# Kernel tuning notes

Measured on AMD Instinct MI355X. Metric: run time of the kernel, lower is better.

## Reference

```python
import jax, jax.numpy as jnp
import numpy as np

N = 16384   # nodes = batch(4) * 64*64 grid
E = 32768   # edges per edge set
L = 32      # LATENT_DIMS
D = 2       # DEPTH (message-passing layers per GNOBlock)
KD = 64     # KERNEL_DIMS
TIN = 10    # TIME_STEPS_IN

def gelu(x):
    return jax.nn.gelu(x, approximate=False)  # torch F.gelu default (erf)

def setup_inputs() -> dict:
    key = jax.random.key(0)
    ks = iter(jax.random.split(key, 64))
    def nrm(shape, s=0.1):
        return jax.random.normal(next(ks), shape, dtype=jnp.float32) * s
    def ridx():
        return jax.random.randint(next(ks), (2, E), 0, N)
    inp = {
        'nodes': nrm((N, TIN), 1.0),
        'grid': jax.random.uniform(next(ks), (N, 2), dtype=jnp.float32),
    }
    for nm in ['11', '12', '22', '23', '33', '32', '21']:
        inp[f'edge_index_{nm}'] = ridx()
    for nm in ['11', '12', '22', '23', '33', '32', '21']:
        inp[f'edge_attr_{nm}'] = nrm((E, 5), 1.0)
    inp['batch_size'] = 4
    inp['image_size'] = 64
    # projector MLP: in_dims=TIN+2 -> hidden L//2 -> L
    inp['proj_w1'] = nrm((TIN + 2, L // 2)); inp['proj_b1'] = jnp.zeros((L // 2,), jnp.float32)
    inp['proj_w2'] = nrm((L // 2, L));       inp['proj_b2'] = jnp.zeros((L,), jnp.float32)
    # decoder MLP: L -> L//2 -> 1
    inp['dec_w1'] = nrm((L, L // 2)); inp['dec_b1'] = jnp.zeros((L // 2,), jnp.float32)
    inp['dec_w2'] = nrm((L // 2, 1)); inp['dec_b2'] = jnp.zeros((1,), jnp.float32)
    # 7 GNOBlocks x D layers: edge kernel MLP (5 -> KD -> L*L) + node linear (L -> L)
    inp['kw1'] = nrm((7, D, 5, KD));      inp['kb1'] = jnp.zeros((7, D, KD), jnp.float32)
    inp['kw2'] = nrm((7, D, KD, L * L));  inp['kb2'] = jnp.zeros((7, D, L * L), jnp.float32)
    inp['lw'] = nrm((7, D, L, L));        inp['lb'] = jnp.zeros((7, D, L), jnp.float32)
    return inp

def _mlp(x, w1, b1, w2, b2):
    return gelu(x @ w1 + b1) @ w2 + b2

def _gno_block(i, x, eidx, eattr, kw1, kb1, kw2, kb2, lw, lb):
    src, dst = eidx[0], eidx[1]
    n = x.shape[0]
    deg = jax.ops.segment_sum(jnp.ones_like(dst, x.dtype), dst, num_segments=n)
    inv_deg = jnp.where(deg > 0, 1.0 / jnp.maximum(deg, 1.0), 0.0)[:, None]
    for d in range(kw1.shape[1]):
        # edge-conditioned kernel: [E, L, L]
        k = _mlp(eattr, kw1[i, d], kb1[i, d], kw2[i, d], kb2[i, d]).reshape(-1, x.shape[1], x.shape[1])
        msg = jnp.einsum('eio,ei->eo', k, x[src])            # gather + per-edge matvec
        agg = jax.ops.segment_sum(msg, dst, num_segments=n) * inv_deg  # scatter-mean
        x = gelu(x @ lw[i, d] + lb[i, d] + agg)              # root linear + activation
    return x

def reference(nodes, grid, edge_index_11, edge_index_12, edge_index_22, edge_index_23,
              edge_index_33, edge_index_32, edge_index_21, edge_attr_11, edge_attr_12,
              edge_attr_22, edge_attr_23, edge_attr_33, edge_attr_32, edge_attr_21,
              batch_size, image_size, proj_w1, proj_b1, proj_w2, proj_b2,
              dec_w1, dec_b1, dec_w2, dec_b2, kw1, kb1, kw2, kb2, lw, lb):
    x = jnp.concatenate([nodes, grid], axis=-1)
    x = gelu(_mlp(x, proj_w1, proj_b1, proj_w2, proj_b2))
    # block param index order matches init order: k11,k22,k33,k12,k23,k32,k21
    n11 = _gno_block(0, x, edge_index_11, edge_attr_11, kw1, kb1, kw2, kb2, lw, lb)
    n12 = _gno_block(3, x, edge_index_12, edge_attr_12, kw1, kb1, kw2, kb2, lw, lb)
    n22 = _gno_block(1, n12, edge_index_22, edge_attr_22, kw1, kb1, kw2, kb2, lw, lb)
    n23 = _gno_block(4, n12, edge_index_23, edge_attr_23, kw1, kb1, kw2, kb2, lw, lb)
    n33 = _gno_block(2, n23, edge_index_33, edge_attr_33, kw1, kb1, kw2, kb2, lw, lb)
    n32 = _gno_block(5, n33, edge_index_32, edge_attr_32, kw1, kb1, kw2, kb2, lw, lb)
    n21 = _gno_block(6, n32 + n22, edge_index_21, edge_attr_21, kw1, kb1, kw2, kb2, lw, lb)
    out = _mlp(n21 + n11, dec_w1, dec_b1, dec_w2, dec_b2)
    return out
```

## Files before the change

kernel.cpp:

```cpp
#include <hip/hip_runtime.h>

#define Nn 16384
#define Ee 32768
#define NL (Nn * 32)

typedef _Float16 hf16;
typedef _Float16 half8 __attribute__((ext_vector_type(8)));
typedef float f32x16 __attribute__((ext_vector_type(16)));

__device__ __forceinline__ float gelu_f(float x) {
    return 0.5f * x * (1.0f + erff(x * 0.7071067811865476f));
}

__device__ __forceinline__ f32x16 zero16() {
    f32x16 v;
#pragma unroll
    for (int r = 0; r < 16; ++r) v[r] = 0.0f;
    return v;
}

__global__ __launch_bounds__(256) void proj_kernel(
    const float* __restrict__ nodes, const float* __restrict__ grid2,
    const float* __restrict__ w1, const float* __restrict__ b1,
    const float* __restrict__ w2, const float* __restrict__ b2,
    float* __restrict__ x0, int* __restrict__ deg_i, int* __restrict__ cursor)
{
    const int n = blockIdx.x * 256 + threadIdx.x;
    float in[12];
#pragma unroll
    for (int j = 0; j < 10; ++j) in[j] = nodes[n * 10 + j];
    in[10] = grid2[n * 2 + 0];
    in[11] = grid2[n * 2 + 1];
    float h[16];
#pragma unroll
    for (int j = 0; j < 16; ++j) {
        float a = b1[j];
#pragma unroll
        for (int i = 0; i < 12; ++i) a = fmaf(in[i], w1[i * 16 + j], a);
        h[j] = gelu_f(a);
    }
#pragma unroll
    for (int o = 0; o < 32; ++o) {
        float a = b2[o];
#pragma unroll
        for (int j = 0; j < 16; ++j) a = fmaf(h[j], w2[j * 32 + o], a);
        x0[(size_t)n * 32 + o] = gelu_f(a);
    }
#pragma unroll
    for (int s = 0; s < 7; ++s) { deg_i[s * Nn + n] = 0; cursor[s * Nn + n] = 0; }
}

struct EPtrs { const int* p[7]; };

__global__ __launch_bounds__(256) void count_deg_kernel(EPtrs ei, int* __restrict__ deg_i)
{
    const int t = blockIdx.x * 256 + threadIdx.x;
    const int s = t >> 15;
    const int e = t & (Ee - 1);
    const int dst = ei.p[s][Ee + e];
    atomicAdd(&deg_i[s * Nn + dst], 1);
}

__global__ __launch_bounds__(256) void scan_kernel(const int* __restrict__ deg_i,
                                                   int* __restrict__ off)
{
    const int s = blockIdx.x;
    const int t = threadIdx.x;
    const int* d = deg_i + (size_t)s * Nn;
    int* o = off + (size_t)s * (Nn + 1);
    int local[64];
    int sum = 0;
#pragma unroll
    for (int j = 0; j < 64; ++j) { local[j] = d[t * 64 + j]; sum += local[j]; }
    __shared__ int ps[256];
    ps[t] = sum;
    __syncthreads();
    for (int st = 1; st < 256; st <<= 1) {
        int v = (t >= st) ? ps[t - st] : 0;
        __syncthreads();
        ps[t] += v;
        __syncthreads();
    }
    int base = (t > 0) ? ps[t - 1] : 0;
#pragma unroll
    for (int j = 0; j < 64; ++j) { o[t * 64 + j] = base; base += local[j]; }
    if (t == 255) o[Nn] = base;
}

__global__ __launch_bounds__(256) void rank_kernel(EPtrs ei, const int* __restrict__ off,
                                                   int* __restrict__ cursor,
                                                   int* __restrict__ rank)
{
    const int t = blockIdx.x * 256 + threadIdx.x;
    const int s = t >> 15;
    const int e = t & (Ee - 1);
    const int dst = ei.p[s][Ee + e];
    const int r = off[(size_t)s * (Nn + 1) + dst] + atomicAdd(&cursor[s * Nn + dst], 1);
    rank[(size_t)s * Ee + e] = r;
}

__global__ __launch_bounds__(320) void wprep_kernel(const float* __restrict__ kw2,
                                                    const float* __restrict__ kb2,
                                                    hf16* __restrict__ Wpack)
{
    const int id = blockIdx.x >> 5;
    const int nt = blockIdx.x & 31;
    const int t = threadIdx.x;
    const int ks = t >> 6, lane = t & 63;
    const float* kw2l = kw2 + (size_t)id * 65536;
    const float* kb2l = kb2 + (size_t)id * 1024;
    half8 vh, vl;
#pragma unroll
    for (int j = 0; j < 8; ++j) {
        const int k = ks * 16 + (lane >> 5) * 8 + j;
        float v = 0.0f;
        if (ks < 4) v = kw2l[(size_t)k * 1024 + (lane & 31) * 32 + nt];
        else if (k == 64) v = kb2l[(lane & 31) * 32 + nt];
        const hf16 h = (hf16)v;
        vh[j] = h;
        vl[j] = (hf16)((v - (float)h) * 1024.0f);
    }
    half8* dst = (half8*)(Wpack + ((size_t)(id * 32 + nt) * 10 + ks * 2) * 512);
    dst[0 * 64 + lane] = vh;
    dst[1 * 64 + lane] = vl;
}

__global__ __launch_bounds__(256, 2) void gemm_kernel(
    const float* __restrict__ xa, const float* __restrict__ xb,
    const int* __restrict__ esrc, const int* __restrict__ erank,
    const float* __restrict__ eattr,
    const float* __restrict__ kw1l, const float* __restrict__ kb1l,
    const hf16* __restrict__ WpackL,
    float* __restrict__ msgS)
{
    __shared__ __align__(16) hf16 hLDS[4 * 5 * 2 * 512];
    const int eblk = blockIdx.x >> 1;
    const int hf = blockIdx.x & 1;
    const int t = threadIdx.x, l = t & 63, wv = t >> 6;
    half8* hp8 = (half8*)hLDS;

    {
        const int e_loc = t >> 1;
        const int hpart = t & 1;
        const int mt = e_loc >> 5, colbase = e_loc & 31;
        const int eg = eblk * 128 + e_loc;
        float ea5[5];
#pragma unroll
        for (int j = 0; j < 5; ++j) ea5[j] = eattr[(size_t)eg * 5 + j];
        half8 vh[2][2], vl[2][2];
#pragma unroll
        for (int hh = 0; hh < 32; ++hh) {
            const int h = hpart * 32 + hh;
            float pre = kb1l[h];
#pragma unroll
            for (int j = 0; j < 5; ++j) pre = fmaf(ea5[j], kw1l[j * 64 + h], pre);
            const float H = gelu_f(pre);
            const hf16 hv = (hf16)H;
            vh[hh >> 4][(hh >> 3) & 1][hh & 7] = hv;
            vl[hh >> 4][(hh >> 3) & 1][hh & 7] = (hf16)((H - (float)hv) * 1024.0f);
        }
#pragma unroll
        for (int ksl = 0; ksl < 2; ++ksl)
#pragma unroll
            for (int kh = 0; kh < 2; ++kh) {
                const int f = (mt * 5 + hpart * 2 + ksl) * 2;
                hp8[f * 64 + colbase + kh * 32] = vh[ksl][kh];
                hp8[(f + 1) * 64 + colbase + kh * 32] = vl[ksl][kh];
            }
        if (hpart == 0) {
            half8 oneV, zV;
#pragma unroll
            for (int j = 0; j < 8; ++j) { oneV[j] = (hf16)0.0f; zV[j] = (hf16)0.0f; }
            oneV[0] = (hf16)1.0f;
            const int f4 = (mt * 5 + 4) * 2;
            hp8[f4 * 64 + colbase] = oneV;
            hp8[f4 * 64 + colbase + 32] = zV;
            hp8[(f4 + 1) * 64 + colbase] = zV;
            hp8[(f4 + 1) * 64 + colbase + 32] = zV;
        }
    }

    const int hi = l >> 5;
    const int el = eblk * 128 + wv * 32 + (l & 31);
    const int src = esrc[el];
    const int rk = erank[el];
    float xsr[16];
#pragma unroll
    for (int c = 0; c < 4; ++c) {
        float4 v = *reinterpret_cast<const float4*>(xa + (size_t)src * 32 + c * 8 + hi * 4);
        if (xb) {
            float4 u = *reinterpret_cast<const float4*>(xb + (size_t)src * 32 + c * 8 + hi * 4);
            v.x += u.x; v.y += u.y; v.z += u.z; v.w += u.w;
        }
        xsr[c * 4 + 0] = v.x; xsr[c * 4 + 1] = v.y;
        xsr[c * 4 + 2] = v.z; xsr[c * 4 + 3] = v.w;
    }

    __syncthreads();

    half8 Hh[5], Hl[5];
#pragma unroll
    for (int ks = 0; ks < 5; ++ks) {
        Hh[ks] = hp8[((wv * 5 + ks) * 2 + 0) * 64 + l];
        Hl[ks] = hp8[((wv * 5 + ks) * 2 + 1) * 64 + l];
    }

    float4 p4;
    const hf16* wbase = WpackL + (size_t)hf * 16 * 5120;

#define LOADW(TT, WH, WL) { \
    const half8* wp = (const half8*)(wbase + (size_t)(TT) * 5120); \
    _Pragma("unroll") for (int ks = 0; ks < 5; ++ks) { \
        WH[ks] = wp[(ks * 2 + 0) * 64 + l]; \
        WL[ks] = wp[(ks * 2 + 1) * 64 + l]; } }

#define COMPUTE(TT, WH, WL) { \
    f32x16 ah = zero16(), ax = zero16(); \
    _Pragma("unroll") for (int ks = 0; ks < 5; ++ks) { \
        ah = __builtin_amdgcn_mfma_f32_32x32x16_f16(WH[ks], Hh[ks], ah, 0, 0, 0); \
        ax = __builtin_amdgcn_mfma_f32_32x32x16_f16(WL[ks], Hh[ks], ax, 0, 0, 0); \
        ax = __builtin_amdgcn_mfma_f32_32x32x16_f16(WH[ks], Hl[ks], ax, 0, 0, 0); } \
    float ph = 0.0f, px = 0.0f; \
    _Pragma("unroll") for (int r = 0; r < 16; ++r) { \
        ph = fmaf(ah[r], xsr[r], ph); px = fmaf(ax[r], xsr[r], px); } \
    float p = fmaf(px, 9.765625e-4f, ph); \
    p += __shfl_xor(p, 32); \
    p4[(TT) & 3] = p; \
    if (((TT) & 3) == 3 && l < 32) \
        *reinterpret_cast<float4*>(msgS + (size_t)rk * 32 + hf * 16 + ((TT) - 3)) = p4; }

    half8 WhA[5], WlA[5], WhB[5], WlB[5];
    LOADW(0, WhA, WlA)
#pragma unroll
    for (int g = 0; g < 8; ++g) {
        LOADW(2 * g + 1, WhB, WlB)
        COMPUTE(2 * g, WhA, WlA)
        if (g < 7) LOADW(2 * g + 2, WhA, WlA)
        COMPUTE(2 * g + 1, WhB, WlB)
    }
#undef LOADW
#undef COMPUTE
}

__global__ __launch_bounds__(256) void node_update_kernel(
    const float* __restrict__ xa, const float* __restrict__ xb,
    float* __restrict__ xout, const float* __restrict__ msgS,
    const int* __restrict__ off,
    const float* __restrict__ lw, const float* __restrict__ lb)
{
    __shared__ float lwS[1024];
#pragma unroll
    for (int c = 0; c < 4; ++c) lwS[threadIdx.x + 256 * c] = lw[threadIdx.x + 256 * c];
    __syncthreads();

    const int g = blockIdx.x * 256 + threadIdx.x;
    const int n = g >> 2;
    const int q = g & 3;

    const int b = off[n], e = off[n + 1];
    float sum[8];
#pragma unroll
    for (int oo = 0; oo < 8; ++oo) sum[oo] = 0.0f;
    for (int j = b; j < e; ++j) {
        const float4 m0 = *reinterpret_cast<const float4*>(msgS + (size_t)j * 32 + q * 8);
        const float4 m1 = *reinterpret_cast<const float4*>(msgS + (size_t)j * 32 + q * 8 + 4);
        sum[0] += m0.x; sum[1] += m0.y; sum[2] += m0.z; sum[3] += m0.w;
        sum[4] += m1.x; sum[5] += m1.y; sum[6] += m1.z; sum[7] += m1.w;
    }
    const float inv = (e > b) ? 1.0f / (float)(e - b) : 0.0f;
    float acc[8];
#pragma unroll
    for (int oo = 0; oo < 8; ++oo) acc[oo] = fmaf(sum[oo], inv, lb[q * 8 + oo]);

    float row[32];
#pragma unroll
    for (int i = 0; i < 32; i += 4) {
        float4 v = *reinterpret_cast<const float4*>(xa + (size_t)n * 32 + i);
        if (xb) {
            float4 u = *reinterpret_cast<const float4*>(xb + (size_t)n * 32 + i);
            v.x += u.x; v.y += u.y; v.z += u.z; v.w += u.w;
        }
        row[i + 0] = v.x; row[i + 1] = v.y; row[i + 2] = v.z; row[i + 3] = v.w;
    }
#pragma unroll
    for (int i = 0; i < 32; ++i) {
        const float xi = row[i];
#pragma unroll
        for (int oo = 0; oo < 8; ++oo) acc[oo] = fmaf(xi, lwS[i * 32 + q * 8 + oo], acc[oo]);
    }
    float4 o0, o1;
    o0.x = gelu_f(acc[0]); o0.y = gelu_f(acc[1]); o0.z = gelu_f(acc[2]); o0.w = gelu_f(acc[3]);
    o1.x = gelu_f(acc[4]); o1.y = gelu_f(acc[5]); o1.z = gelu_f(acc[6]); o1.w = gelu_f(acc[7]);
    *reinterpret_cast<float4*>(xout + (size_t)n * 32 + q * 8) = o0;
    *reinterpret_cast<float4*>(xout + (size_t)n * 32 + q * 8 + 4) = o1;
}

__global__ __launch_bounds__(256) void decode_kernel(
    const float* __restrict__ a, const float* __restrict__ b,
    const float* __restrict__ w1, const float* __restrict__ b1,
    const float* __restrict__ w2, const float* __restrict__ b2,
    float* __restrict__ out)
{
    const int n = blockIdx.x * 256 + threadIdx.x;
    float s[32];
#pragma unroll
    for (int i = 0; i < 32; ++i) s[i] = a[(size_t)n * 32 + i] + b[(size_t)n * 32 + i];
    float acc = b2[0];
#pragma unroll
    for (int j = 0; j < 16; ++j) {
        float h = b1[j];
#pragma unroll
        for (int i = 0; i < 32; ++i) h = fmaf(s[i], w1[i * 16 + j], h);
        acc = fmaf(gelu_f(h), w2[j], acc);
    }
    out[n] = acc;
}

extern "C" void kernel_launch(void* const* d_in, const int* in_sizes, int n_in,
                              void* d_out, int out_size, void* d_ws, size_t ws_size,
                              hipStream_t stream)
{
    const float* nodes = (const float*)d_in[0];
    const float* grid2 = (const float*)d_in[1];
    const int* ei[7];
    const float* ea[7];
    for (int s = 0; s < 7; ++s) {
        ei[s] = (const int*)d_in[2 + s];
        ea[s] = (const float*)d_in[9 + s];
    }
    const float* pw1 = (const float*)d_in[18];
    const float* pb1 = (const float*)d_in[19];
    const float* pw2 = (const float*)d_in[20];
    const float* pb2 = (const float*)d_in[21];
    const float* dw1 = (const float*)d_in[22];
    const float* db1 = (const float*)d_in[23];
    const float* dw2 = (const float*)d_in[24];
    const float* db2 = (const float*)d_in[25];
    const float* kw1 = (const float*)d_in[26];
    const float* kb1 = (const float*)d_in[27];
    const float* kw2 = (const float*)d_in[28];
    const float* kb2 = (const float*)d_in[29];
    const float* lw  = (const float*)d_in[30];
    const float* lb  = (const float*)d_in[31];

    float* ws  = (float*)d_ws;
    float* x0   = ws + 0 * (size_t)NL;
    float* n11  = ws + 1 * (size_t)NL;
    float* n12  = ws + 2 * (size_t)NL;
    float* n22  = ws + 3 * (size_t)NL;
    float* n23  = ws + 4 * (size_t)NL;
    float* n33  = ws + 5 * (size_t)NL;
    float* n32  = ws + 6 * (size_t)NL;
    float* n21  = ws + 7 * (size_t)NL;
    float* msgS = ws + 8 * (size_t)NL;
    size_t cur = 8 * (size_t)NL + (size_t)Ee * 32;
    hf16* Wpack = (hf16*)(ws + cur);
    cur += (size_t)14 * 32 * 10 * 512 / 2;
    int* deg_i  = (int*)(ws + cur); cur += (size_t)7 * Nn;
    int* cursor = (int*)(ws + cur); cur += (size_t)7 * Nn;
    int* off    = (int*)(ws + cur); cur += (size_t)7 * (Nn + 1);
    int* rank   = (int*)(ws + cur);

    proj_kernel<<<Nn / 256, 256, 0, stream>>>(nodes, grid2, pw1, pb1, pw2, pb2,
                                              x0, deg_i, cursor);

    EPtrs ep;
    for (int s = 0; s < 7; ++s) ep.p[s] = ei[s];
    count_deg_kernel<<<7 * Ee / 256, 256, 0, stream>>>(ep, deg_i);
    scan_kernel<<<7, 256, 0, stream>>>(deg_i, off);
    rank_kernel<<<7 * Ee / 256, 256, 0, stream>>>(ep, off, cursor, rank);
    wprep_kernel<<<14 * 32, 320, 0, stream>>>(kw2, kb2, Wpack);

    auto layer = [&](int i, int d, int s, const float* xa, const float* xb, float* xo) {
        const int id = i * 2 + d;
        gemm_kernel<<<(Ee / 128) * 2, 256, 0, stream>>>(
            xa, xb, ei[s], rank + (size_t)s * Ee, ea[s],
            kw1 + (size_t)id * 320, kb1 + (size_t)id * 64,
            Wpack + (size_t)id * 32 * 5120, msgS);
        node_update_kernel<<<Nn * 4 / 256, 256, 0, stream>>>(
            xa, xb, xo, msgS, off + (size_t)s * (Nn + 1),
            lw + (size_t)id * 1024, lb + (size_t)id * 32);
    };
    auto gno_block = [&](int i, int s, const float* xa, const float* xb, float* xo) {
        layer(i, 0, s, xa, xb, xo);
        layer(i, 1, s, xo, nullptr, xo);
    };

    gno_block(0, 0, x0,  nullptr, n11);
    gno_block(3, 1, x0,  nullptr, n12);
    gno_block(1, 2, n12, nullptr, n22);
    gno_block(4, 3, n12, nullptr, n23);
    gno_block(2, 4, n23, nullptr, n33);
    gno_block(5, 5, n33, nullptr, n32);
    gno_block(6, 6, n32, n22,     n21);

    decode_kernel<<<Nn / 256, 256, 0, stream>>>(n11, n21, dw1, db1, dw2, db2, (float*)d_out);
}
```

Before: 557.6 us.

## Move kernel-bias term out of edge GEMM into node update via source-sum

The per-edge bias kb2 was previously folded into the MFMA GEMM as a fifth K-slice with a constant-one input. It is now applied per node as mean(x_src)·kb2 inside node_update, using a new dst-sorted source index array built in rank_kernel. This shortens the GEMM K dimension from 80 to 64. The GEMM grid is also split into quarters with a higher occupancy hint. The cost is that node_update now gathers 32 floats of source features per edge, adding memory traffic and register pressure (a 32-float accumulator).

```diff
diff --git a/kernel.cpp b/kernel.cpp
--- a/kernel.cpp
+++ b/kernel.cpp
@@ -89,7 +89,8 @@
 
 __global__ __launch_bounds__(256) void rank_kernel(EPtrs ei, const int* __restrict__ off,
                                                    int* __restrict__ cursor,
-                                                   int* __restrict__ rank)
+                                                   int* __restrict__ rank,
+                                                   int* __restrict__ srcS)
 {
     const int t = blockIdx.x * 256 + threadIdx.x;
     const int s = t >> 15;
@@ -97,10 +98,10 @@
     const int dst = ei.p[s][Ee + e];
     const int r = off[(size_t)s * (Nn + 1) + dst] + atomicAdd(&cursor[s * Nn + dst], 1);
     rank[(size_t)s * Ee + e] = r;
-}
-
-__global__ __launch_bounds__(320) void wprep_kernel(const float* __restrict__ kw2,
-                                                    const float* __restrict__ kb2,
+    srcS[(size_t)s * Ee + r] = ei.p[s][e];
+}
+
+__global__ __launch_bounds__(256) void wprep_kernel(const float* __restrict__ kw2,
                                                     hf16* __restrict__ Wpack)
 {
     const int id = blockIdx.x >> 5;
@@ -108,24 +109,21 @@
     const int t = threadIdx.x;
     const int ks = t >> 6, lane = t & 63;
     const float* kw2l = kw2 + (size_t)id * 65536;
-    const float* kb2l = kb2 + (size_t)id * 1024;
     half8 vh, vl;
 #pragma unroll
     for (int j = 0; j < 8; ++j) {
         const int k = ks * 16 + (lane >> 5) * 8 + j;
-        float v = 0.0f;
-        if (ks < 4) v = kw2l[(size_t)k * 1024 + (lane & 31) * 32 + nt];
-        else if (k == 64) v = kb2l[(lane & 31) * 32 + nt];
+        const float v = kw2l[(size_t)k * 1024 + (lane & 31) * 32 + nt];
         const hf16 h = (hf16)v;
         vh[j] = h;
         vl[j] = (hf16)((v - (float)h) * 1024.0f);
     }
-    half8* dst = (half8*)(Wpack + ((size_t)(id * 32 + nt) * 10 + ks * 2) * 512);
+    half8* dst = (half8*)(Wpack + ((size_t)(id * 32 + nt) * 8 + ks * 2) * 512);
     dst[0 * 64 + lane] = vh;
     dst[1 * 64 + lane] = vl;
 }
 
-__global__ __launch_bounds__(256, 2) void gemm_kernel(
+__global__ __launch_bounds__(256, 3) void gemm_kernel(
     const float* __restrict__ xa, const float* __restrict__ xb,
     const int* __restrict__ esrc, const int* __restrict__ erank,
     const float* __restrict__ eattr,
@@ -133,9 +131,9 @@
     const hf16* __restrict__ WpackL,
     float* __restrict__ msgS)
 {
-    __shared__ __align__(16) hf16 hLDS[4 * 5 * 2 * 512];
-    const int eblk = blockIdx.x >> 1;
-    const int hf = blockIdx.x & 1;
+    __shared__ __align__(16) hf16 hLDS[4 * 4 * 2 * 512];
+    const int eblk = blockIdx.x >> 2;
+    const int qid = blockIdx.x & 3;
     const int t = threadIdx.x, l = t & 63, wv = t >> 6;
     half8* hp8 = (half8*)hLDS;
 
@@ -163,21 +161,10 @@
         for (int ksl = 0; ksl < 2; ++ksl)
 #pragma unroll
             for (int kh = 0; kh < 2; ++kh) {
-                const int f = (mt * 5 + hpart * 2 + ksl) * 2;
+                const int f = (mt * 4 + hpart * 2 + ksl) * 2;
                 hp8[f * 64 + colbase + kh * 32] = vh[ksl][kh];
                 hp8[(f + 1) * 64 + colbase + kh * 32] = vl[ksl][kh];
             }
-        if (hpart == 0) {
-            half8 oneV, zV;
-#pragma unroll
-            for (int j = 0; j < 8; ++j) { oneV[j] = (hf16)0.0f; zV[j] = (hf16)0.0f; }
-            oneV[0] = (hf16)1.0f;
-            const int f4 = (mt * 5 + 4) * 2;
-            hp8[f4 * 64 + colbase] = oneV;
-            hp8[f4 * 64 + colbase + 32] = zV;
-            hp8[(f4 + 1) * 64 + colbase] = zV;
-            hp8[(f4 + 1) * 64 + colbase + 32] = zV;
-        }
     }
 
     const int hi = l >> 5;
@@ -198,25 +185,25 @@
 
     __syncthreads();
 
-    half8 Hh[5], Hl[5];
-#pragma unroll
-    for (int ks = 0; ks < 5; ++ks) {
-        Hh[ks] = hp8[((wv * 5 + ks) * 2 + 0) * 64 + l];
-        Hl[ks] = hp8[((wv * 5 + ks) * 2 + 1) * 64 + l];
+    half8 Hh[4], Hl[4];
+#pragma unroll
+    for (int ks = 0; ks < 4; ++ks) {
+        Hh[ks] = hp8[((wv * 4 + ks) * 2 + 0) * 64 + l];
+        Hl[ks] = hp8[((wv * 4 + ks) * 2 + 1) * 64 + l];
     }
 
     float4 p4;
-    const hf16* wbase = WpackL + (size_t)hf * 16 * 5120;
+    const hf16* wbase = WpackL + (size_t)qid * 8 * 4096;
 
 #define LOADW(TT, WH, WL) { \
-    const half8* wp = (const half8*)(wbase + (size_t)(TT) * 5120); \
-    _Pragma("unroll") for (int ks = 0; ks < 5; ++ks) { \
+    const half8* wp = (const half8*)(wbase + (size_t)(TT) * 4096); \
+    _Pragma("unroll") for (int ks = 0; ks < 4; ++ks) { \
         WH[ks] = wp[(ks * 2 + 0) * 64 + l]; \
         WL[ks] = wp[(ks * 2 + 1) * 64 + l]; } }
 
 #define COMPUTE(TT, WH, WL) { \
     f32x16 ah = zero16(), ax = zero16(); \
-    _Pragma("unroll") for (int ks = 0; ks < 5; ++ks) { \
+    _Pragma("unroll") for (int ks = 0; ks < 4; ++ks) { \
         ah = __builtin_amdgcn_mfma_f32_32x32x16_f16(WH[ks], Hh[ks], ah, 0, 0, 0); \
         ax = __builtin_amdgcn_mfma_f32_32x32x16_f16(WL[ks], Hh[ks], ax, 0, 0, 0); \
         ax = __builtin_amdgcn_mfma_f32_32x32x16_f16(WH[ks], Hl[ks], ax, 0, 0, 0); } \
@@ -227,15 +214,15 @@
     p += __shfl_xor(p, 32); \
     p4[(TT) & 3] = p; \
     if (((TT) & 3) == 3 && l < 32) \
-        *reinterpret_cast<float4*>(msgS + (size_t)rk * 32 + hf * 16 + ((TT) - 3)) = p4; }
-
-    half8 WhA[5], WlA[5], WhB[5], WlB[5];
+        *reinterpret_cast<float4*>(msgS + (size_t)rk * 32 + qid * 8 + ((TT) - 3)) = p4; }
+
+    half8 WhA[4], WlA[4], WhB[4], WlB[4];
     LOADW(0, WhA, WlA)
 #pragma unroll
-    for (int g = 0; g < 8; ++g) {
+    for (int g = 0; g < 4; ++g) {
         LOADW(2 * g + 1, WhB, WlB)
         COMPUTE(2 * g, WhA, WlA)
-        if (g < 7) LOADW(2 * g + 2, WhA, WlA)
+        if (g < 3) LOADW(2 * g + 2, WhA, WlA)
         COMPUTE(2 * g + 1, WhB, WlB)
     }
 #undef LOADW
@@ -245,12 +232,17 @@
 __global__ __launch_bounds__(256) void node_update_kernel(
     const float* __restrict__ xa, const float* __restrict__ xb,
     float* __restrict__ xout, const float* __restrict__ msgS,
-    const int* __restrict__ off,
-    const float* __restrict__ lw, const float* __restrict__ lb)
+    const int* __restrict__ off, const int* __restrict__ srcS,
+    const float* __restrict__ lw, const float* __restrict__ lb,
+    const float* __restrict__ kb2l)
 {
     __shared__ float lwS[1024];
-#pragma unroll
-    for (int c = 0; c < 4; ++c) lwS[threadIdx.x + 256 * c] = lw[threadIdx.x + 256 * c];
+    __shared__ float kbS[1024];
+#pragma unroll
+    for (int c = 0; c < 4; ++c) {
+        lwS[threadIdx.x + 256 * c] = lw[threadIdx.x + 256 * c];
+        kbS[threadIdx.x + 256 * c] = kb2l[threadIdx.x + 256 * c];
+    }
     __syncthreads();
 
     const int g = blockIdx.x * 256 + threadIdx.x;
@@ -259,13 +251,27 @@
 
     const int b = off[n], e = off[n + 1];
     float sum[8];
+    float xsum[32];
 #pragma unroll
     for (int oo = 0; oo < 8; ++oo) sum[oo] = 0.0f;
+#pragma unroll
+    for (int i = 0; i < 32; ++i) xsum[i] = 0.0f;
     for (int j = b; j < e; ++j) {
         const float4 m0 = *reinterpret_cast<const float4*>(msgS + (size_t)j * 32 + q * 8);
         const float4 m1 = *reinterpret_cast<const float4*>(msgS + (size_t)j * 32 + q * 8 + 4);
         sum[0] += m0.x; sum[1] += m0.y; sum[2] += m0.z; sum[3] += m0.w;
         sum[4] += m1.x; sum[5] += m1.y; sum[6] += m1.z; sum[7] += m1.w;
+        const int src = srcS[j];
+#pragma unroll
+        for (int c = 0; c < 8; ++c) {
+            float4 v = *reinterpret_cast<const float4*>(xa + (size_t)src * 32 + c * 4);
+            if (xb) {
+                float4 u = *reinterpret_cast<const float4*>(xb + (size_t)src * 32 + c * 4);
+                v.x += u.x; v.y += u.y; v.z += u.z; v.w += u.w;
+            }
+            xsum[c * 4 + 0] += v.x; xsum[c * 4 + 1] += v.y;
+            xsum[c * 4 + 2] += v.z; xsum[c * 4 + 3] += v.w;
+        }
     }
     const float inv = (e > b) ? 1.0f / (float)(e - b) : 0.0f;
     float acc[8];
@@ -285,8 +291,12 @@
 #pragma unroll
     for (int i = 0; i < 32; ++i) {
         const float xi = row[i];
-#pragma unroll
-        for (int oo = 0; oo < 8; ++oo) acc[oo] = fmaf(xi, lwS[i * 32 + q * 8 + oo], acc[oo]);
+        const float xm = xsum[i] * inv;
+#pragma unroll
+        for (int oo = 0; oo < 8; ++oo) {
+            acc[oo] = fmaf(xi, lwS[i * 32 + q * 8 + oo], acc[oo]);
+            acc[oo] = fmaf(xm, kbS[i * 32 + q * 8 + oo], acc[oo]);
+        }
     }
     float4 o0, o1;
     o0.x = gelu_f(acc[0]); o0.y = gelu_f(acc[1]); o0.z = gelu_f(acc[2]); o0.w = gelu_f(acc[3]);
@@ -355,11 +365,12 @@
     float* msgS = ws + 8 * (size_t)NL;
     size_t cur = 8 * (size_t)NL + (size_t)Ee * 32;
     hf16* Wpack = (hf16*)(ws + cur);
-    cur += (size_t)14 * 32 * 10 * 512 / 2;
+    cur += (size_t)14 * 32 * 8 * 512 / 2;
     int* deg_i  = (int*)(ws + cur); cur += (size_t)7 * Nn;
     int* cursor = (int*)(ws + cur); cur += (size_t)7 * Nn;
     int* off    = (int*)(ws + cur); cur += (size_t)7 * (Nn + 1);
-    int* rank   = (int*)(ws + cur);
+    int* rank   = (int*)(ws + cur); cur += (size_t)7 * Ee;
+    int* srcS   = (int*)(ws + cur);
 
     proj_kernel<<<Nn / 256, 256, 0, stream>>>(nodes, grid2, pw1, pb1, pw2, pb2,
                                               x0, deg_i, cursor);
@@ -368,18 +379,18 @@
     for (int s = 0; s < 7; ++s) ep.p[s] = ei[s];
     count_deg_kernel<<<7 * Ee / 256, 256, 0, stream>>>(ep, deg_i);
     scan_kernel<<<7, 256, 0, stream>>>(deg_i, off);
-    rank_kernel<<<7 * Ee / 256, 256, 0, stream>>>(ep, off, cursor, rank);
-    wprep_kernel<<<14 * 32, 320, 0, stream>>>(kw2, kb2, Wpack);
+    rank_kernel<<<7 * Ee / 256, 256, 0, stream>>>(ep, off, cursor, rank, srcS);
+    wprep_kernel<<<14 * 32, 256, 0, stream>>>(kw2, Wpack);
 
     auto layer = [&](int i, int d, int s, const float* xa, const float* xb, float* xo) {
         const int id = i * 2 + d;
-        gemm_kernel<<<(Ee / 128) * 2, 256, 0, stream>>>(
+        gemm_kernel<<<(Ee / 128) * 4, 256, 0, stream>>>(
             xa, xb, ei[s], rank + (size_t)s * Ee, ea[s],
             kw1 + (size_t)id * 320, kb1 + (size_t)id * 64,
-            Wpack + (size_t)id * 32 * 5120, msgS);
+            Wpack + (size_t)id * 32 * 4096, msgS);
         node_update_kernel<<<Nn * 4 / 256, 256, 0, stream>>>(
-            xa, xb, xo, msgS, off + (size_t)s * (Nn + 1),
-            lw + (size_t)id * 1024, lb + (size_t)id * 32);
+            xa, xb, xo, msgS, off + (size_t)s * (Nn + 1), srcS + (size_t)s * Ee,
+            lw + (size_t)id * 1024, lb + (size_t)id * 32, kb2 + (size_t)id * 1024);
     };
     auto gno_block = [&](int i, int s, const float* xa, const float* xb, float* xo) {
         layer(i, 0, s, xa, xb, xo);
```

Result: slower. 1.015 ms (+82.0%).

## Restructure node update to wave-per-node with coalesced message reads

Applied to the files above, without the earlier changes.

The node update kernel now assigns one wavefront to each node (four nodes per wave), with lanes mapped to output channels and the two half-waves splitting edges and input channels, combined via shuffles. This makes message reads coalesced per edge row instead of each thread striding through float4 chunks, and spreads the 32x32 linear across lanes. The gemm kernel drops its occupancy hint of 2 from launch_bounds, which may change register allocation. The offset buffer also gains one element of padding.

```diff
diff --git a/kernel.cpp b/kernel.cpp
--- a/kernel.cpp
+++ b/kernel.cpp
@@ -18,6 +18,8 @@
     for (int r = 0; r < 16; ++r) v[r] = 0.0f;
     return v;
 }
+
+struct EPtrs { const int* p[7]; };
 
 __global__ __launch_bounds__(256) void proj_kernel(
     const float* __restrict__ nodes, const float* __restrict__ grid2,
@@ -49,8 +51,6 @@
 #pragma unroll
     for (int s = 0; s < 7; ++s) { deg_i[s * Nn + n] = 0; cursor[s * Nn + n] = 0; }
 }
-
-struct EPtrs { const int* p[7]; };
 
 __global__ __launch_bounds__(256) void count_deg_kernel(EPtrs ei, int* __restrict__ deg_i)
 {
@@ -125,9 +125,9 @@
     dst[1 * 64 + lane] = vl;
 }
 
-__global__ __launch_bounds__(256, 2) void gemm_kernel(
+__global__ __launch_bounds__(256) void g11(
     const float* __restrict__ xa, const float* __restrict__ xb,
-    const int* __restrict__ esrc, const int* __restrict__ erank,
+    const int* __restrict__ eidx, const int* __restrict__ erank,
     const float* __restrict__ eattr,
     const float* __restrict__ kw1l, const float* __restrict__ kb1l,
     const hf16* __restrict__ WpackL,
@@ -182,7 +182,7 @@
 
     const int hi = l >> 5;
     const int el = eblk * 128 + wv * 32 + (l & 31);
-    const int src = esrc[el];
+    const int src = eidx[el];
     const int rk = erank[el];
     float xsr[16];
 #pragma unroll
@@ -242,7 +242,7 @@
 #undef COMPUTE
 }
 
-__global__ __launch_bounds__(256) void node_update_kernel(
+__global__ __launch_bounds__(256) void nu11(
     const float* __restrict__ xa, const float* __restrict__ xb,
     float* __restrict__ xout, const float* __restrict__ msgS,
     const int* __restrict__ off,
@@ -253,46 +253,38 @@
     for (int c = 0; c < 4; ++c) lwS[threadIdx.x + 256 * c] = lw[threadIdx.x + 256 * c];
     __syncthreads();
 
-    const int g = blockIdx.x * 256 + threadIdx.x;
-    const int n = g >> 2;
-    const int q = g & 3;
-
-    const int b = off[n], e = off[n + 1];
-    float sum[8];
-#pragma unroll
-    for (int oo = 0; oo < 8; ++oo) sum[oo] = 0.0f;
-    for (int j = b; j < e; ++j) {
-        const float4 m0 = *reinterpret_cast<const float4*>(msgS + (size_t)j * 32 + q * 8);
-        const float4 m1 = *reinterpret_cast<const float4*>(msgS + (size_t)j * 32 + q * 8 + 4);
-        sum[0] += m0.x; sum[1] += m0.y; sum[2] += m0.z; sum[3] += m0.w;
-        sum[4] += m1.x; sum[5] += m1.y; sum[6] += m1.z; sum[7] += m1.w;
-    }
-    const float inv = (e > b) ? 1.0f / (float)(e - b) : 0.0f;
-    float acc[8];
-#pragma unroll
-    for (int oo = 0; oo < 8; ++oo) acc[oo] = fmaf(sum[oo], inv, lb[q * 8 + oo]);
-
-    float row[32];
-#pragma unroll
-    for (int i = 0; i < 32; i += 4) {
-        float4 v = *reinterpret_cast<const float4*>(xa + (size_t)n * 32 + i);
-        if (xb) {
-            float4 u = *reinterpret_cast<const float4*>(xb + (size_t)n * 32 + i);
-            v.x += u.x; v.y += u.y; v.z += u.z; v.w += u.w;
-        }
-        row[i + 0] = v.x; row[i + 1] = v.y; row[i + 2] = v.z; row[i + 3] = v.w;
-    }
-#pragma unroll
-    for (int i = 0; i < 32; ++i) {
-        const float xi = row[i];
-#pragma unroll
-        for (int oo = 0; oo < 8; ++oo) acc[oo] = fmaf(xi, lwS[i * 32 + q * 8 + oo], acc[oo]);
-    }
-    float4 o0, o1;
-    o0.x = gelu_f(acc[0]); o0.y = gelu_f(acc[1]); o0.z = gelu_f(acc[2]); o0.w = gelu_f(acc[3]);
-    o1.x = gelu_f(acc[4]); o1.y = gelu_f(acc[5]); o1.z = gelu_f(acc[6]); o1.w = gelu_f(acc[7]);
-    *reinterpret_cast<float4*>(xout + (size_t)n * 32 + q * 8) = o0;
-    *reinterpret_cast<float4*>(xout + (size_t)n * 32 + q * 8 + 4) = o1;
+    const int t = threadIdx.x, l = t & 63, wv = t >> 6;
+    const int o = l & 31, jj = l >> 5;
+
+#pragma unroll
+    for (int it = 0; it < 4; ++it) {
+        const int n = blockIdx.x * 16 + wv * 4 + it;
+        const int b = off[n], e = off[n + 1];
+        float sum = 0.0f;
+        for (int j = b + jj; j < e; j += 2) {
+            sum += msgS[(size_t)j * 32 + o];
+        }
+        sum += __shfl_xor(sum, 32);
+        const float inv = (e > b) ? 1.0f / (float)(e - b) : 0.0f;
+
+        float part = 0.0f;
+#pragma unroll
+        for (int c = 0; c < 4; ++c) {
+            float4 v = *reinterpret_cast<const float4*>(xa + (size_t)n * 32 + jj * 16 + c * 4);
+            if (xb) {
+                float4 u = *reinterpret_cast<const float4*>(xb + (size_t)n * 32 + jj * 16 + c * 4);
+                v.x += u.x; v.y += u.y; v.z += u.z; v.w += u.w;
+            }
+            part = fmaf(v.x, lwS[(jj * 16 + c * 4 + 0) * 32 + o], part);
+            part = fmaf(v.y, lwS[(jj * 16 + c * 4 + 1) * 32 + o], part);
+            part = fmaf(v.z, lwS[(jj * 16 + c * 4 + 2) * 32 + o], part);
+            part = fmaf(v.w, lwS[(jj * 16 + c * 4 + 3) * 32 + o], part);
+        }
+        part += __shfl_xor(part, 32);
+
+        const float acc = fmaf(sum, inv, lb[o]) + part;
+        if (l < 32) xout[(size_t)n * 32 + o] = gelu_f(acc);
+    }
 }
 
 __global__ __launch_bounds__(256) void decode_kernel(
@@ -358,7 +350,7 @@
     cur += (size_t)14 * 32 * 10 * 512 / 2;
     int* deg_i  = (int*)(ws + cur); cur += (size_t)7 * Nn;
     int* cursor = (int*)(ws + cur); cur += (size_t)7 * Nn;
-    int* off    = (int*)(ws + cur); cur += (size_t)7 * (Nn + 1);
+    int* off    = (int*)(ws + cur); cur += (size_t)7 * (Nn + 1) + 1;
     int* rank   = (int*)(ws + cur);
 
     proj_kernel<<<Nn / 256, 256, 0, stream>>>(nodes, grid2, pw1, pb1, pw2, pb2,
@@ -373,11 +365,11 @@
 
     auto layer = [&](int i, int d, int s, const float* xa, const float* xb, float* xo) {
         const int id = i * 2 + d;
-        gemm_kernel<<<(Ee / 128) * 2, 256, 0, stream>>>(
+        g11<<<(Ee / 128) * 2, 256, 0, stream>>>(
             xa, xb, ei[s], rank + (size_t)s * Ee, ea[s],
             kw1 + (size_t)id * 320, kb1 + (size_t)id * 64,
             Wpack + (size_t)id * 32 * 5120, msgS);
-        node_update_kernel<<<Nn * 4 / 256, 256, 0, stream>>>(
+        nu11<<<Nn / 16, 256, 0, stream>>>(
             xa, xb, xo, msgS, off + (size_t)s * (Nn + 1),
             lw + (size_t)id * 1024, lb + (size_t)id * 32);
     };
```

Result: slower. 610.8 us (+9.5%).
